# Optimization experiments

Measured on AMD Instinct MI355X. Metric: run time of the kernel, lower is better.

The kernel has to match this reference:

```python
import jax, jax.numpy as jnp
import numpy as np

H = 256  # hidden_size


def setup_inputs() -> dict:
    key = jax.random.key(0)
    k1, k2, k3 = jax.random.split(key, 3)
    N, L, V, Emb = 128, 2048, 32000, 256
    X = jax.random.randint(k1, (N, L), 0, V, dtype=jnp.int64)
    E = jax.random.normal(k2, (V, Emb), dtype=jnp.float32) * 0.02
    W_w = jax.random.normal(k3, (4 * H, H + Emb), dtype=jnp.float32) * (1.0 / np.sqrt(H + Emb))
    W_b = jnp.zeros((4 * H,), dtype=jnp.float32)
    return {"X": X, "E": E, "W_w": W_w, "W_b": W_b}


def reference(X, E, W_w, W_b):
    # X: (N, L) int token ids
    N, L = X.shape
    Xe = E[X]                      # (N, L, Emb) embedded sequence
    Xe_t = jnp.swapaxes(Xe, 0, 1)  # (L, N, Emb) scan over time

    def step(carry, x_t):
        H_t, C_t = carry
        hx = jnp.concatenate([H_t, x_t], axis=1)           # (N, H+Emb)
        G = hx @ W_w.T + W_b                               # (N, 4H)
        F_g = jax.nn.sigmoid(G[:, :H])
        # NOTE: original code computes I = sigmoid(G[:, H:2H]) but never uses it
        O_g = jax.nn.sigmoid(G[:, 2 * H:3 * H])
        H_tmp = jnp.tanh(G[:, 3 * H:4 * H])
        # Faithful to source: C_t = F*C + O*H_tmp (uses O, not I)
        C_new = F_g * C_t + O_g * H_tmp
        H_new = O_g * jnp.tanh(C_new)
        return (H_new, C_new), None

    init = (jnp.zeros((N, H), Xe.dtype), jnp.zeros((N, H), Xe.dtype))
    (H_last, _), _ = jax.lax.scan(step, init, Xe_t)
    return H_last
```

## Files before the change

### kernel.cpp

```cpp
#include <hip/hip_runtime.h>
#include <hip/hip_bf16.h>

#define N_B   128
#define L_SEQ 2048
#define H_DIM 256
#define EMB   256
#define G3    768
#define G4    1024
#define WROW  512
#define V_SZ  32000


typedef unsigned short ushort_t;
typedef unsigned int   uint_t;

using f32x4  = __attribute__((ext_vector_type(4))) float;
using bf16x8 = __attribute__((ext_vector_type(8))) short;
using h2_t   = __attribute__((ext_vector_type(2))) _Float16;
using f16x8  = __attribute__((ext_vector_type(8))) _Float16;
using ushort4_t = __attribute__((ext_vector_type(4))) ushort_t;
using u32x4  = __attribute__((ext_vector_type(4))) uint_t;

__device__ __forceinline__ float bf2f(ushort_t u) {
  union { uint_t u; float f; } x; x.u = ((uint_t)u) << 16; return x.f;
}
__device__ __forceinline__ ushort_t f2bf(float f) {
  union { float f; uint_t u; } x; x.f = f;
  return (ushort_t)((x.u + 0x7fffu + ((x.u >> 16) & 1u)) >> 16);
}
__device__ __forceinline__ float rcp_f(float x) {
#if __has_builtin(__builtin_amdgcn_rcpf)
  return __builtin_amdgcn_rcpf(x);
#else
  return 1.0f / x;
#endif
}
__device__ __forceinline__ float clampf(float x, float lo, float hi) {
  return fminf(fmaxf(x, lo), hi);
}
__device__ __forceinline__ float sigmoid_f(float x) {
  x = clampf(x, -30.f, 30.f);
  return rcp_f(1.0f + __expf(-x));
}
__device__ __forceinline__ float tanh_f(float x) {
  x = clampf(x, -15.f, 15.f);
  float e = __expf(-2.0f * x);
  return (1.0f - e) * rcp_f(1.0f + e);
}
__device__ __forceinline__ h2_t bfpair_to_h2(uint_t u) {
  union { uint_t u; float f; } lo, hi;
  lo.u = u << 16;
  hi.u = u & 0xffff0000u;
  h2_t r; r.x = (_Float16)lo.f; r.y = (_Float16)hi.f; return r;
}

__device__ __forceinline__ int gmap(int g) { return (g < 256) ? g : g + 256; }

#define FENCE_V8(A) asm volatile("" :                                         \
  "+v"((A)[0]), "+v"((A)[1]), "+v"((A)[2]), "+v"((A)[3]),                     \
  "+v"((A)[4]), "+v"((A)[5]), "+v"((A)[6]), "+v"((A)[7]))

__global__ void dtype_probe(const uint_t* __restrict__ Ed,
                            const uint_t* __restrict__ Xd,
                            const uint_t* __restrict__ Wd,
                            uint_t* __restrict__ flags) {
  if (threadIdx.x != 0 || blockIdx.x != 0) return;
  int saneE = 0, saneW = 0;
  for (int i = 0; i < 256; ++i) {
    uint_t le = Ed[i] & 0xffffu, ee = (le >> 7) & 0xffu;
    if (ee == 0u || (ee >= 90u && ee <= 126u)) saneE++;
    uint_t lw = Wd[i] & 0xffffu, ew = (lw >> 7) & 0xffu;
    if (ew == 0u || (ew >= 90u && ew <= 126u)) saneW++;
  }
  uint_t nz = 0u;
  for (int i = 0; i < 128; ++i) nz |= Xd[2 * i + 1];
  flags[0] = (saneE < 192) ? 1u : 0u;
  flags[1] = (nz == 0u) ? 1u : 0u;
  flags[2] = (saneW < 192) ? 1u : 0u;
}

__global__ __launch_bounds__(256) void eg_gemm(const void* __restrict__ Ein,
                                               const void* __restrict__ Wwin,
                                               const void* __restrict__ Wbin,
                                               _Float16* __restrict__ Eg,
                                               const uint_t* __restrict__ flags) {
  __shared__ __align__(16) ushort_t At[16][264];
  const int tid = threadIdx.x;
  const int v0  = blockIdx.x * 16;
  const uint_t ef32 = flags[0];
  const uint_t wf32 = flags[2];

  if (!ef32) {
    const ushort_t* E = (const ushort_t*)Ein;
#pragma unroll
    for (int i = 0; i < 2; ++i) {
      int idx = tid + i * 256;
      int row = idx >> 5, seg = idx & 31;
      const uint4* src = (const uint4*)(E + (size_t)(v0 + row) * EMB + seg * 8);
      *(uint4*)&At[row][seg * 8] = *src;
    }
  } else {
    const float* Ef = (const float*)Ein;
#pragma unroll
    for (int i = 0; i < 4; ++i) {
      int idx = tid + i * 256;
      int row = idx >> 6, seg = idx & 63;
      float4 v = *(const float4*)(Ef + (size_t)(v0 + row) * EMB + seg * 4);
      ushort4_t s;
      s.x = f2bf(v.x); s.y = f2bf(v.y); s.z = f2bf(v.z); s.w = f2bf(v.w);
      *(ushort4_t*)&At[row][seg * 4] = s;
    }
  }
  __syncthreads();

  const int lane = tid & 63, wv = tid >> 6;
  const int m = lane & 15, q = lane >> 4;

  f32x4 acc[12];
#pragma unroll
  for (int nt = 0; nt < 12; ++nt) acc[nt] = f32x4{0.f, 0.f, 0.f, 0.f};

  if (!wf32) {
    const ushort_t* Ww = (const ushort_t*)Wwin;
#pragma unroll
    for (int kt = 0; kt < 8; ++kt) {
      bf16x8 a = *(const bf16x8*)&At[m][kt * 32 + q * 8];
#pragma unroll
      for (int nt = 0; nt < 12; ++nt) {
        int g  = wv * 192 + nt * 16 + m;
        int gr = gmap(g);
        const bf16x8* bp =
            (const bf16x8*)(Ww + (size_t)gr * WROW + EMB + kt * 32 + q * 8);
        acc[nt] = __builtin_amdgcn_mfma_f32_16x16x32_bf16(a, *bp, acc[nt], 0, 0, 0);
      }
    }
  } else {
    const float* Wf = (const float*)Wwin;
#pragma unroll
    for (int kt = 0; kt < 8; ++kt) {
      bf16x8 a = *(const bf16x8*)&At[m][kt * 32 + q * 8];
#pragma unroll
      for (int nt = 0; nt < 12; ++nt) {
        int g  = wv * 192 + nt * 16 + m;
        int gr = gmap(g);
        const float* wp = Wf + (size_t)gr * WROW + EMB + kt * 32 + q * 8;
        float4 w0 = *(const float4*)(wp);
        float4 w1 = *(const float4*)(wp + 4);
        bf16x8 b;
        b[0] = (short)f2bf(w0.x); b[1] = (short)f2bf(w0.y);
        b[2] = (short)f2bf(w0.z); b[3] = (short)f2bf(w0.w);
        b[4] = (short)f2bf(w1.x); b[5] = (short)f2bf(w1.y);
        b[6] = (short)f2bf(w1.z); b[7] = (short)f2bf(w1.w);
        acc[nt] = __builtin_amdgcn_mfma_f32_16x16x32_bf16(a, b, acc[nt], 0, 0, 0);
      }
    }
  }

#pragma unroll
  for (int nt = 0; nt < 12; ++nt) {
    int g  = wv * 192 + nt * 16 + m;
    int gr = gmap(g);
    float bias = wf32 ? ((const float*)Wbin)[gr] : bf2f(((const ushort_t*)Wbin)[gr]);
#pragma unroll
    for (int j = 0; j < 4; ++j) {
      int v = v0 + q * 4 + j;
      Eg[(size_t)v * G3 + g] = (_Float16)(acc[nt][j] + bias);
    }
  }
}

__global__ __launch_bounds__(1024)
void lstm_rec_mfma(const int* __restrict__ Xi,
                   const void* __restrict__ Wwin,
                   const _Float16* __restrict__ Eg,
                   float* __restrict__ out,
                   const uint_t* __restrict__ flags) {
  __shared__ __align__(16) _Float16 hbuf[2][256];
  __shared__ __align__(16) float    Gbuf[G3];
  const int tid  = threadIdx.x;
  const int lane = tid & 63;
  const int w    = tid >> 6;
  const int q    = lane >> 4;
  const int rr   = lane & 15;
  const int n    = blockIdx.x;
  const uint_t wf32 = flags[2];
  const uint_t x64  = flags[1];

  u32x4 wAq[24];
  if (!wf32) {
    const ushort_t* Wb16 = (const ushort_t*)Wwin;
#pragma unroll
    for (int m = 0; m < 3; ++m) {
      const int grow = (w * 3 + m) * 16 + rr;
      const int wr   = gmap(grow);
      const ushort_t* rp = Wb16 + (size_t)wr * WROW + q * 8;
#pragma unroll
      for (int kt = 0; kt < 8; ++kt) {
        u32x4 v = *(const u32x4*)(rp + kt * 32);
        u32x4 t;
#pragma unroll
        for (int cc = 0; cc < 4; ++cc)
          t[cc] = __builtin_bit_cast(uint_t, bfpair_to_h2(v[cc]));
        wAq[m * 8 + kt] = t;
      }
    }
  } else {
    const float* Wf = (const float*)Wwin;
#pragma unroll
    for (int m = 0; m < 3; ++m) {
      const int grow = (w * 3 + m) * 16 + rr;
      const int wr   = gmap(grow);
      const float* rp = Wf + (size_t)wr * WROW + q * 8;
#pragma unroll
      for (int kt = 0; kt < 8; ++kt) {
        const float* pp = rp + kt * 32;
        float4 a = *(const float4*)(pp);
        float4 b = *(const float4*)(pp + 4);
        h2_t p0, p1, p2, p3;
        p0.x = (_Float16)a.x; p0.y = (_Float16)a.y;
        p1.x = (_Float16)a.z; p1.y = (_Float16)a.w;
        p2.x = (_Float16)b.x; p2.y = (_Float16)b.y;
        p3.x = (_Float16)b.z; p3.y = (_Float16)b.w;
        u32x4 t;
        t[0] = __builtin_bit_cast(uint_t, p0);
        t[1] = __builtin_bit_cast(uint_t, p1);
        t[2] = __builtin_bit_cast(uint_t, p2);
        t[3] = __builtin_bit_cast(uint_t, p3);
        wAq[m * 8 + kt] = t;
      }
    }
  }
  FENCE_V8(wAq); FENCE_V8(wAq + 8); FENCE_V8(wAq + 16);

  if (tid < 256) hbuf[0][tid] = (_Float16)0.f;

  float c = 0.f, hlast = 0.f;
  const size_t xbase = (size_t)n * L_SEQ;

  float pxF = 0.f, pxO = 0.f, pxT = 0.f;
  if (tid < 256) {
    int tok0 = x64 ? Xi[xbase * 2] : Xi[xbase];
    if ((uint_t)tok0 >= (uint_t)V_SZ) tok0 = 0;
    const _Float16* e = Eg + (size_t)tok0 * G3 + tid;
    pxF = (float)e[0]; pxO = (float)e[256]; pxT = (float)e[512];
  }

  int cur = 0;
  for (int t = 0; t < L_SEQ; ++t) {
    __syncthreads();

    float nF = 0.f, nO = 0.f, nT = 0.f;
    if (tid < 256) {
      int tp = (t + 1 < L_SEQ) ? (t + 1) : (L_SEQ - 1);
      int tok = x64 ? Xi[(xbase + tp) * 2] : Xi[xbase + tp];
      if ((uint_t)tok >= (uint_t)V_SZ) tok = 0;
      const _Float16* e = Eg + (size_t)tok * G3 + tid;
      nF = (float)e[0]; nO = (float)e[256]; nT = (float)e[512];
    }

    f32x4 acc0 = f32x4{0.f, 0.f, 0.f, 0.f};
    f32x4 acc1 = f32x4{0.f, 0.f, 0.f, 0.f};
    f32x4 acc2 = f32x4{0.f, 0.f, 0.f, 0.f};
#pragma unroll
    for (int kt = 0; kt < 8; ++kt) {
      f16x8 b = *(const f16x8*)&hbuf[cur][kt * 32 + q * 8];
      acc0 = __builtin_amdgcn_mfma_f32_16x16x32_f16(
          __builtin_bit_cast(f16x8, wAq[kt]),      b, acc0, 0, 0, 0);
      acc1 = __builtin_amdgcn_mfma_f32_16x16x32_f16(
          __builtin_bit_cast(f16x8, wAq[8 + kt]),  b, acc1, 0, 0, 0);
      acc2 = __builtin_amdgcn_mfma_f32_16x16x32_f16(
          __builtin_bit_cast(f16x8, wAq[16 + kt]), b, acc2, 0, 0, 0);
    }

    if (rr == 0) {
      *(f32x4*)&Gbuf[(w * 3 + 0) * 16 + q * 4] = acc0;
      *(f32x4*)&Gbuf[(w * 3 + 1) * 16 + q * 4] = acc1;
      *(f32x4*)&Gbuf[(w * 3 + 2) * 16 + q * 4] = acc2;
    }
    __syncthreads();

    if (tid < 256) {
      float aF = Gbuf[tid]       + pxF;
      float aO = Gbuf[256 + tid] + pxO;
      float aT = Gbuf[512 + tid] + pxT;
      float Fg = sigmoid_f(aF);
      float Og = sigmoid_f(aO);
      float Tg = tanh_f(aT);
      c = Fg * c + Og * Tg;
      float hv2 = Og * tanh_f(c);
      hlast = hv2;
      hbuf[cur ^ 1][tid] = (_Float16)hv2;
      pxF = nF; pxO = nO; pxT = nT;
    }
    cur ^= 1;
  }

  if (tid < 256) out[(size_t)n * H_DIM + tid] = hlast;
}

extern "C" void kernel_launch(void* const* d_in, const int* in_sizes, int n_in,
                              void* d_out, int out_size, void* d_ws, size_t ws_size,
                              hipStream_t stream) {
  const void* X  = d_in[0];
  const void* E  = d_in[1];
  const void* Ww = d_in[2];
  const void* Wb = d_in[3];
  for (int i = 0; i < n_in && i < 4; ++i) {
    switch (in_sizes[i]) {
      case N_B * L_SEQ: X  = d_in[i]; break;
      case V_SZ * EMB:  E  = d_in[i]; break;
      case G4 * WROW:   Ww = d_in[i]; break;
      case G4:          Wb = d_in[i]; break;
      default: break;
    }
  }
  float* out = (float*)d_out;

  uint_t*   flags = (uint_t*)d_ws;
  _Float16* Eg    = (_Float16*)((char*)d_ws + 256);

  dtype_probe<<<dim3(1), dim3(64), 0, stream>>>(
      (const uint_t*)E, (const uint_t*)X, (const uint_t*)Ww, flags);
  eg_gemm<<<dim3(V_SZ / 16), dim3(256), 0, stream>>>(E, Ww, Wb, Eg, flags);
  lstm_rec_mfma<<<dim3(N_B), dim3(1024), 0, stream>>>(
      (const int*)X, Ww, Eg, out, flags);
}
```

Baseline: 2.966 ms.

## Align gate rows per wave so MFMA outputs feed cell update directly

Each wave now owns 16 hidden units and loads the matching F, O and T weight rows, so every gate accumulator for a hidden unit lands in the same lane. The gate values are read from the MFMA accumulators with a register select, which removes the Gbuf shared-memory round trip and one __syncthreads per timestep. In exchange the elementwise update runs on lanes with rr<4 spread across all waves instead of on the first 256 threads, which adds divergence within each wave.

```diff
diff --git a/kernel.cpp b/kernel.cpp
--- a/kernel.cpp
+++ b/kernel.cpp
@@ -55,6 +55,14 @@
 }
 
 __device__ __forceinline__ int gmap(int g) { return (g < 256) ? g : g + 256; }
+
+__device__ __forceinline__ float sel4(f32x4 v, int r) {
+  float x = v[0];
+  x = (r == 1) ? v[1] : x;
+  x = (r == 2) ? v[2] : x;
+  x = (r == 3) ? v[3] : x;
+  return x;
+}
 
 #define FENCE_V8(A) asm volatile("" :                                         \
   "+v"((A)[0]), "+v"((A)[1]), "+v"((A)[2]), "+v"((A)[3]),                     \
@@ -176,7 +184,6 @@
                    float* __restrict__ out,
                    const uint_t* __restrict__ flags) {
   __shared__ __align__(16) _Float16 hbuf[2][256];
-  __shared__ __align__(16) float    Gbuf[G3];
   const int tid  = threadIdx.x;
   const int lane = tid & 63;
   const int w    = tid >> 6;
@@ -185,48 +192,51 @@
   const int n    = blockIdx.x;
   const uint_t wf32 = flags[2];
   const uint_t x64  = flags[1];
+  const int jc   = w * 16 + q * 4 + (rr & 3);
 
   u32x4 wAq[24];
-  if (!wf32) {
-    const ushort_t* Wb16 = (const ushort_t*)Wwin;
-#pragma unroll
-    for (int m = 0; m < 3; ++m) {
-      const int grow = (w * 3 + m) * 16 + rr;
-      const int wr   = gmap(grow);
-      const ushort_t* rp = Wb16 + (size_t)wr * WROW + q * 8;
-#pragma unroll
-      for (int kt = 0; kt < 8; ++kt) {
-        u32x4 v = *(const u32x4*)(rp + kt * 32);
-        u32x4 t;
-#pragma unroll
-        for (int cc = 0; cc < 4; ++cc)
-          t[cc] = __builtin_bit_cast(uint_t, bfpair_to_h2(v[cc]));
-        wAq[m * 8 + kt] = t;
+  {
+    const int rowF = 16 * w + rr;
+    const int rowO = 512 + 16 * w + rr;
+    const int rowT = 768 + 16 * w + rr;
+    const int rows[3] = {rowF, rowO, rowT};
+    if (!wf32) {
+      const ushort_t* Wb16 = (const ushort_t*)Wwin;
+#pragma unroll
+      for (int m = 0; m < 3; ++m) {
+        const ushort_t* rp = Wb16 + (size_t)rows[m] * WROW + q * 8;
+#pragma unroll
+        for (int kt = 0; kt < 8; ++kt) {
+          u32x4 v = *(const u32x4*)(rp + kt * 32);
+          u32x4 s;
+#pragma unroll
+          for (int cc = 0; cc < 4; ++cc)
+            s[cc] = __builtin_bit_cast(uint_t, bfpair_to_h2(v[cc]));
+          wAq[m * 8 + kt] = s;
+        }
       }
-    }
-  } else {
-    const float* Wf = (const float*)Wwin;
-#pragma unroll
-    for (int m = 0; m < 3; ++m) {
-      const int grow = (w * 3 + m) * 16 + rr;
-      const int wr   = gmap(grow);
-      const float* rp = Wf + (size_t)wr * WROW + q * 8;
-#pragma unroll
-      for (int kt = 0; kt < 8; ++kt) {
-        const float* pp = rp + kt * 32;
-        float4 a = *(const float4*)(pp);
-        float4 b = *(const float4*)(pp + 4);
-        h2_t p0, p1, p2, p3;
-        p0.x = (_Float16)a.x; p0.y = (_Float16)a.y;
-        p1.x = (_Float16)a.z; p1.y = (_Float16)a.w;
-        p2.x = (_Float16)b.x; p2.y = (_Float16)b.y;
-        p3.x = (_Float16)b.z; p3.y = (_Float16)b.w;
-        u32x4 t;
-        t[0] = __builtin_bit_cast(uint_t, p0);
-        t[1] = __builtin_bit_cast(uint_t, p1);
-        t[2] = __builtin_bit_cast(uint_t, p2);
-        t[3] = __builtin_bit_cast(uint_t, p3);
-        wAq[m * 8 + kt] = t;
+    } else {
+      const float* Wf = (const float*)Wwin;
+#pragma unroll
+      for (int m = 0; m < 3; ++m) {
+        const float* rp = Wf + (size_t)rows[m] * WROW + q * 8;
+#pragma unroll
+        for (int kt = 0; kt < 8; ++kt) {
+          const float* pp = rp + kt * 32;
+          float4 a = *(const float4*)(pp);
+          float4 b = *(const float4*)(pp + 4);
+          h2_t p0, p1, p2, p3;
+          p0.x = (_Float16)a.x; p0.y = (_Float16)a.y;
+          p1.x = (_Float16)a.z; p1.y = (_Float16)a.w;
+          p2.x = (_Float16)b.x; p2.y = (_Float16)b.y;
+          p3.x = (_Float16)b.z; p3.y = (_Float16)b.w;
+          u32x4 s;
+          s[0] = __builtin_bit_cast(uint_t, p0);
+          s[1] = __builtin_bit_cast(uint_t, p1);
+          s[2] = __builtin_bit_cast(uint_t, p2);
+          s[3] = __builtin_bit_cast(uint_t, p3);
+          wAq[m * 8 + kt] = s;
+        }
       }
     }
   }
@@ -238,10 +248,10 @@
   const size_t xbase = (size_t)n * L_SEQ;
 
   float pxF = 0.f, pxO = 0.f, pxT = 0.f;
-  if (tid < 256) {
+  if (rr < 4) {
     int tok0 = x64 ? Xi[xbase * 2] : Xi[xbase];
     if ((uint_t)tok0 >= (uint_t)V_SZ) tok0 = 0;
-    const _Float16* e = Eg + (size_t)tok0 * G3 + tid;
+    const _Float16* e = Eg + (size_t)tok0 * G3 + jc;
     pxF = (float)e[0]; pxO = (float)e[256]; pxT = (float)e[512];
   }
 
@@ -250,52 +260,45 @@
     __syncthreads();
 
     float nF = 0.f, nO = 0.f, nT = 0.f;
-    if (tid < 256) {
+    if (rr < 4) {
       int tp = (t + 1 < L_SEQ) ? (t + 1) : (L_SEQ - 1);
       int tok = x64 ? Xi[(xbase + tp) * 2] : Xi[xbase + tp];
       if ((uint_t)tok >= (uint_t)V_SZ) tok = 0;
-      const _Float16* e = Eg + (size_t)tok * G3 + tid;
+      const _Float16* e = Eg + (size_t)tok * G3 + jc;
       nF = (float)e[0]; nO = (float)e[256]; nT = (float)e[512];
     }
 
-    f32x4 acc0 = f32x4{0.f, 0.f, 0.f, 0.f};
-    f32x4 acc1 = f32x4{0.f, 0.f, 0.f, 0.f};
-    f32x4 acc2 = f32x4{0.f, 0.f, 0.f, 0.f};
+    f32x4 aF4 = f32x4{0.f, 0.f, 0.f, 0.f};
+    f32x4 aO4 = f32x4{0.f, 0.f, 0.f, 0.f};
+    f32x4 aT4 = f32x4{0.f, 0.f, 0.f, 0.f};
 #pragma unroll
     for (int kt = 0; kt < 8; ++kt) {
       f16x8 b = *(const f16x8*)&hbuf[cur][kt * 32 + q * 8];
-      acc0 = __builtin_amdgcn_mfma_f32_16x16x32_f16(
-          __builtin_bit_cast(f16x8, wAq[kt]),      b, acc0, 0, 0, 0);
-      acc1 = __builtin_amdgcn_mfma_f32_16x16x32_f16(
-          __builtin_bit_cast(f16x8, wAq[8 + kt]),  b, acc1, 0, 0, 0);
-      acc2 = __builtin_amdgcn_mfma_f32_16x16x32_f16(
-          __builtin_bit_cast(f16x8, wAq[16 + kt]), b, acc2, 0, 0, 0);
-    }
-
-    if (rr == 0) {
-      *(f32x4*)&Gbuf[(w * 3 + 0) * 16 + q * 4] = acc0;
-      *(f32x4*)&Gbuf[(w * 3 + 1) * 16 + q * 4] = acc1;
-      *(f32x4*)&Gbuf[(w * 3 + 2) * 16 + q * 4] = acc2;
-    }
-    __syncthreads();
-
-    if (tid < 256) {
-      float aF = Gbuf[tid]       + pxF;
-      float aO = Gbuf[256 + tid] + pxO;
-      float aT = Gbuf[512 + tid] + pxT;
+      aF4 = __builtin_amdgcn_mfma_f32_16x16x32_f16(
+          __builtin_bit_cast(f16x8, wAq[kt]),      b, aF4, 0, 0, 0);
+      aO4 = __builtin_amdgcn_mfma_f32_16x16x32_f16(
+          __builtin_bit_cast(f16x8, wAq[8 + kt]),  b, aO4, 0, 0, 0);
+      aT4 = __builtin_amdgcn_mfma_f32_16x16x32_f16(
+          __builtin_bit_cast(f16x8, wAq[16 + kt]), b, aT4, 0, 0, 0);
+    }
+
+    if (rr < 4) {
+      float aF = sel4(aF4, rr) + pxF;
+      float aO = sel4(aO4, rr) + pxO;
+      float aT = sel4(aT4, rr) + pxT;
       float Fg = sigmoid_f(aF);
       float Og = sigmoid_f(aO);
       float Tg = tanh_f(aT);
       c = Fg * c + Og * Tg;
       float hv2 = Og * tanh_f(c);
       hlast = hv2;
-      hbuf[cur ^ 1][tid] = (_Float16)hv2;
+      hbuf[cur ^ 1][jc] = (_Float16)hv2;
       pxF = nF; pxO = nO; pxT = nT;
     }
     cur ^= 1;
   }
 
-  if (tid < 256) out[(size_t)n * H_DIM + tid] = hlast;
+  if (rr < 4) out[(size_t)n * H_DIM + jc] = hlast;
 }
 
 extern "C" void kernel_launch(void* const* d_in, const int* in_sizes, int n_in,
```

After: 3.291 ms. 11.0% more time.
